# Kernel tuning notes

Hardware: AMD Instinct MI355X
Metric: run time of the kernel (lower is better)

The kernel has to match this reference:

```python
import jax, jax.numpy as jnp
import numpy as np

STATE_DIM = 128
ACT_DIM = 32
ENC_K = 10   # encoder_spine_dim
DEC_K = 10   # decoder_dim
H0, H1 = 2048, 2048
BATCH = 16384
MAX_ACTION = 1.0
STD0 = 0.3872983346207417  # sqrt(0.15)


def setup_inputs() -> dict:
    key = jax.random.key(0)
    ks = jax.random.split(key, 10)
    state = jax.random.normal(ks[0], (BATCH, STATE_DIM), dtype=jnp.float32)
    # encoder params: mean linspace over mean_range, std constant
    mean_enc = jnp.broadcast_to(jnp.linspace(-3.0, 3.0, ENC_K, dtype=jnp.float32),
                                (1, STATE_DIM, ENC_K))
    std_enc = jnp.full((1, STATE_DIM, ENC_K), STD0, dtype=jnp.float32)
    def lin(k, fan_in, fan_out):
        bound = 1.0 / np.sqrt(fan_in)
        k1, k2 = jax.random.split(k)
        W = jax.random.uniform(k1, (fan_out, fan_in), jnp.float32, -bound, bound)
        b = jax.random.uniform(k2, (fan_out,), jnp.float32, -bound, bound)
        return W, b
    W1, b1 = lin(ks[1], STATE_DIM * ENC_K, H0)
    W2, b2 = lin(ks[2], H0, H1)
    W3, b3 = lin(ks[3], H1, ACT_DIM * DEC_K)
    # grouped conv1d: weight [act_dim, 1, dec_k], bias [act_dim]
    bound = 1.0 / np.sqrt(DEC_K)
    Wd = jax.random.uniform(ks[4], (ACT_DIM, 1, DEC_K), jnp.float32, -bound, bound)
    bd = jax.random.uniform(ks[5], (ACT_DIM,), jnp.float32, -bound, bound)
    return {"state": state, "mean_enc": mean_enc, "std_enc": std_enc,
            "W1": W1, "b1": b1, "W2": W2, "b2": b2, "W3": W3, "b3": b3,
            "Wd": Wd, "bd": bd}


def reference(state, mean_enc, std_enc, W1, b1, W2, b2, W3, b3, Wd, bd):
    # Population-coding encoder: sigmoid((obs - mean)/std), flattened
    spine = jax.nn.sigmoid((state[:, :, None] - mean_enc) / std_enc)  # [B, D, K]
    spine = spine.reshape(state.shape[0], -1)                         # [B, D*K]
    a = jax.nn.relu(spine @ W1.T + b1)
    a = jax.nn.relu(a @ W2.T + b2)
    a = a @ W3.T + b3                                                 # [B, A*Kd]
    d = a.reshape(-1, ACT_DIM, DEC_K)                                 # [B, A, Kd]
    # grouped Conv1d with kernel == length => per-channel dot product
    raw = jnp.einsum('bak,ak->ba', d, Wd[:, 0, :]) + bd               # [B, A]
    return MAX_ACTION * jnp.tanh(raw)
```

## Files before the change

kernel.cpp:

```cpp
#include <hip/hip_runtime.h>
#include <hip/hip_bf16.h>
#include <stdint.h>

#define BATCH   16384
#define SDIM    128
#define ENCK    10
#define ADIM    32
#define DECK    10
#define HID     2048
#define KSPINE  1280

typedef __bf16 bf16x8 __attribute__((ext_vector_type(8)));
typedef float  f32x4  __attribute__((ext_vector_type(4)));

typedef __attribute__((address_space(1))) const void kGlobalVoid;
typedef __attribute__((address_space(3))) void       kLdsVoid;

__device__ __forceinline__ unsigned short f2b(float f) {
  union { float f; unsigned u; } v; v.f = f;
  unsigned r = v.u + 0x7fffu + ((v.u >> 16) & 1u);
  return (unsigned short)(r >> 16);
}

__global__ void f2b_kernel(const float* __restrict__ in, unsigned* __restrict__ out, int n2) {
  int i = blockIdx.x * blockDim.x + threadIdx.x;
  if (i >= n2) return;
  float2 v = reinterpret_cast<const float2*>(in)[i];
  out[i] = (unsigned)f2b(v.x) | ((unsigned)f2b(v.y) << 16);
}

__global__ __launch_bounds__(256) void encoder_kernel(const float* __restrict__ state,
                               const float* __restrict__ mean,
                               const float* __restrict__ stdv,
                               unsigned* __restrict__ spine) {
  int idx = blockIdx.x * 256 + threadIdx.x;
  int idx1 = (int)(((long long)idx * 0x66666667LL) >> 33);
  int kk = idx - idx1 * 5;
  int d  = idx1 & (SDIM - 1);
  float x = state[idx1];
  int mi = d * ENCK + kk * 2;
  float m0 = mean[mi], m1 = mean[mi + 1];
  float s0 = stdv[mi], s1 = stdv[mi + 1];
  float v0 = 1.f / (1.f + __expf((m0 - x) / s0));
  float v1 = 1.f / (1.f + __expf((m1 - x) / s1));
  spine[idx] = (unsigned)f2b(v0) | ((unsigned)f2b(v1) << 16);
}

__global__ void weff_kernel(const float* __restrict__ W3, const float* __restrict__ Wd,
                            unsigned short* __restrict__ Weff) {
  int idx = blockIdx.x * 256 + threadIdx.x;
  int a = idx >> 11, j = idx & 2047;
  float s = 0.f;
#pragma unroll
  for (int k = 0; k < DECK; ++k)
    s += Wd[a * DECK + k] * W3[(size_t)(a * DECK + k) * HID + j];
  Weff[idx] = f2b(s);
}

__global__ void beff_kernel(const float* __restrict__ b3, const float* __restrict__ Wd,
                            const float* __restrict__ bd, float* __restrict__ beff) {
  int a = threadIdx.x;
  if (a >= ADIM) return;
  float s = bd[a];
#pragma unroll
  for (int k = 0; k < DECK; ++k) s += Wd[a * DECK + k] * b3[a * DECK + k];
  beff[a] = s;
}


#define A0B 0
#define B0B 32768
#define A1B 65536
#define B1B 98304

#define FENCE asm volatile("" ::: "memory")

#define STAGE(BASEPTR, R0A, R0B, LDS0, LDS1, KT)                                             \
  __builtin_amdgcn_global_load_lds((kGlobalVoid*)((BASEPTR) + (size_t)((R0A) + rs) * K + (KT) + ce), \
                                   (kLdsVoid*)(smem + (LDS0) + t * 16), 16, 0, 0);           \
  __builtin_amdgcn_global_load_lds((kGlobalVoid*)((BASEPTR) + (size_t)((R0B) + rs) * K + (KT) + ce), \
                                   (kLdsVoid*)(smem + (LDS1) + t * 16), 16, 0, 0);

#define DS_AF(DST, ABASE, MPN)                                                               \
  _Pragma("unroll")                                                                          \
  for (int j2 = 0; j2 < 2; ++j2) {                                                           \
    _Pragma("unroll")                                                                        \
    for (int ks = 0; ks < 2; ++ks) {                                                         \
      int rowl = wr * 128 + (MPN) * 32 + j2 * 16 + lr;                                       \
      DST[j2][ks] = *reinterpret_cast<const bf16x8*>(                                        \
          smem + (ABASE) + rowl * 128 + ((((ks) << 6) | (kh << 4)) ^ swz));                  \
    }                                                                                        \
  }

#define DS_B2(DST, NP, BBASE)                                                                \
  _Pragma("unroll")                                                                          \
  for (int ks = 0; ks < 2; ++ks) {                                                           \
    int rowl = wc * 64 + (NP) * 16 + lr;                                                     \
    DST[NP][ks] = *reinterpret_cast<const bf16x8*>(                                          \
        smem + (BBASE) + rowl * 128 + ((((ks) << 6) | (kh << 4)) ^ swz));                    \
  }

#define DS_BF(DST, BBASE)                                                                    \
  _Pragma("unroll")                                                                          \
  for (int n = 0; n < 4; ++n) {                                                              \
    _Pragma("unroll")                                                                        \
    for (int ks = 0; ks < 2; ++ks) {                                                         \
      int rowl = wc * 64 + n * 16 + lr;                                                      \
      DST[n][ks] = *reinterpret_cast<const bf16x8*>(                                         \
          smem + (BBASE) + rowl * 128 + ((((ks) << 6) | (kh << 4)) ^ swz));                  \
    }                                                                                        \
  }

#define MFMA16(MP, AF, BF)                                                                   \
  _Pragma("unroll")                                                                          \
  for (int j2 = 0; j2 < 2; ++j2)                                                             \
    _Pragma("unroll")                                                                        \
    for (int n = 0; n < 4; ++n)                                                              \
      _Pragma("unroll")                                                                      \
      for (int ks = 0; ks < 2; ++ks)                                                         \
        acc[(MP) * 2 + j2][n] = __builtin_amdgcn_mfma_f32_16x16x32_bf16(                     \
            AF[j2][ks], BF[n][ks], acc[(MP) * 2 + j2][n], 0, 0, 0);

#define SGB_PHASE                                                                            \
  __builtin_amdgcn_sched_group_barrier(0x8, 2, 0);                                           \
  __builtin_amdgcn_sched_group_barrier(0x100, 1, 0);                                         \
  __builtin_amdgcn_sched_group_barrier(0x8, 2, 0);                                           \
  __builtin_amdgcn_sched_group_barrier(0x100, 1, 0);                                         \
  __builtin_amdgcn_sched_group_barrier(0x20, 2, 0);                                          \
  __builtin_amdgcn_sched_group_barrier(0x8, 3, 0);                                           \
  __builtin_amdgcn_sched_group_barrier(0x100, 1, 0);                                         \
  __builtin_amdgcn_sched_group_barrier(0x8, 3, 0);                                           \
  __builtin_amdgcn_sched_group_barrier(0x100, 1, 0);                                         \
  __builtin_amdgcn_sched_group_barrier(0x8, 3, 0);                                           \
  __builtin_amdgcn_sched_group_barrier(0x100, 1, 0);                                         \
  __builtin_amdgcn_sched_group_barrier(0x8, 3, 0);                                           \
  __builtin_amdgcn_sched_group_barrier(0x100, 1, 0);

#define VM_NONE
#define VM2 asm volatile("s_waitcnt vmcnt(2)" ::: "memory"); __builtin_amdgcn_sched_barrier(0);
#define VM6 asm volatile("s_waitcnt vmcnt(6)" ::: "memory"); __builtin_amdgcn_sched_barrier(0);

#define PH(MP, AF_C, AF_N, BF_C, BF_N, NXT_A, NXT_MP, BBASE_N, VMW, STG)                     \
  do {                                                                                       \
    asm volatile("s_waitcnt lgkmcnt(0)" ::: "memory");                                       \
    __builtin_amdgcn_sched_barrier(0);                                                       \
    VMW                                                                                      \
    __builtin_amdgcn_s_setprio(1);                                                           \
    MFMA16(MP, AF_C, BF_C);                                                                  \
    __builtin_amdgcn_s_setprio(0);                                                           \
    DS_AF(AF_N, NXT_A, NXT_MP);                                                              \
    DS_B2(BF_N, MP, BBASE_N);                                                                \
    STG;                                                                                     \
    SGB_PHASE;                                                                               \
    FENCE;                                                                                   \
    __builtin_amdgcn_s_barrier();                                                            \
  } while (0)

__global__ __launch_bounds__(512, 2) void gemm256(
    const unsigned short* __restrict__ A,
    const unsigned short* __restrict__ Bw,
    const float* __restrict__ bias,
    unsigned short* __restrict__ Cout,
    int K, int NI) {
  __shared__ char smem[131072];

  const int t    = threadIdx.x;
  const int lane = t & 63;
  const int w    = t >> 6;
  const int wr   = w >> 2;
  const int wc   = w & 3;
  const int lr   = lane & 15;
  const int kh   = lane >> 4;
  const int swz  = (lr & 7) << 4;
  const int rs   = t >> 3;
  const int ce   = ((t & 7) ^ (rs & 7)) << 3;

  const int bid = blockIdx.x;
  const int xcd = bid & 7, idx = bid >> 3;
  const int row0 = (xcd * 8 + (idx >> 3)) * 256;
  const int col0 = (idx & 7) * 256;

  f32x4 acc[8][4];
#pragma unroll
  for (int m = 0; m < 8; ++m)
#pragma unroll
    for (int n = 0; n < 4; ++n)
      acc[m][n] = (f32x4){0.f, 0.f, 0.f, 0.f};

  bf16x8 afc[2][2], afn[2][2], bfA[4][2], bfB[4][2];

  STAGE(Bw, col0 + 0,   col0 + 64,  B0B + 0,     B0B + 8192,  0);
  STAGE(Bw, col0 + 128, col0 + 192, B0B + 16384, B0B + 24576, 0);
  STAGE(A,  row0 + 0,   row0 + 128, A0B + 0,     A0B + 16384, 0);
  STAGE(A,  row0 + 64,  row0 + 192, A0B + 8192,  A0B + 24576, 0);
  STAGE(Bw, col0 + 0,   col0 + 64,  B1B + 0,     B1B + 8192,  64);
  STAGE(Bw, col0 + 128, col0 + 192, B1B + 16384, B1B + 24576, 64);
  STAGE(A,  row0 + 0,   row0 + 128, A1B + 0,     A1B + 16384, 64);
  asm volatile("s_waitcnt vmcnt(0)" ::: "memory");
  FENCE;
  __builtin_amdgcn_s_barrier();
  DS_AF(afc, A0B, 0);
  DS_BF(bfA, B0B);

  for (int i = 0; i < NI; ++i) {
    int kt0 = i << 7;
    int kt1 = kt0 + 64;
    int kt2 = kt0 + 128; if (kt2 >= K) kt2 -= K;
    int kt3 = kt0 + 192; if (kt3 >= K) kt3 -= K;

    PH(0, afc, afn, bfA, bfB, A0B, 1, B1B, VM2,
       STAGE(A,  row0 + 64,  row0 + 192, A1B + 8192,  A1B + 24576, kt1));
    PH(1, afn, afc, bfA, bfB, A0B, 2, B1B, VM_NONE,
       STAGE(Bw, col0 + 0,   col0 + 64,  B0B + 0,     B0B + 8192,  kt2));
    PH(2, afc, afn, bfA, bfB, A0B, 3, B1B, VM_NONE,
       STAGE(Bw, col0 + 128, col0 + 192, B0B + 16384, B0B + 24576, kt2));
    PH(3, afn, afc, bfA, bfB, A1B, 0, B1B, VM6,
       STAGE(A,  row0 + 0,   row0 + 128, A0B + 0,     A0B + 16384, kt2));
    PH(0, afc, afn, bfB, bfA, A1B, 1, B0B, VM2,
       STAGE(A,  row0 + 64,  row0 + 192, A0B + 8192,  A0B + 24576, kt2));
    PH(1, afn, afc, bfB, bfA, A1B, 2, B0B, VM_NONE,
       STAGE(Bw, col0 + 0,   col0 + 64,  B1B + 0,     B1B + 8192,  kt3));
    PH(2, afc, afn, bfB, bfA, A1B, 3, B0B, VM_NONE,
       STAGE(Bw, col0 + 128, col0 + 192, B1B + 16384, B1B + 24576, kt3));
    PH(3, afn, afc, bfB, bfA, A0B, 0, B0B, VM6,
       STAGE(A,  row0 + 0,   row0 + 128, A1B + 0,     A1B + 16384, kt3));
  }

#pragma unroll
  for (int m = 0; m < 8; ++m) {
    int gr0 = row0 + wr * 128 + m * 16 + kh * 4;
#pragma unroll
    for (int n = 0; n < 4; ++n) {
      int gc = col0 + wc * 64 + n * 16 + lr;
      float bv = bias[gc];
#pragma unroll
      for (int v = 0; v < 4; ++v) {
        float val = fmaxf(acc[m][n][v] + bv, 0.f);
        Cout[(size_t)(gr0 + v) * 2048 + gc] = f2b(val);
      }
    }
  }
}

__global__ __launch_bounds__(256) void gemm_skinny(
    const unsigned short* __restrict__ A,
    const unsigned short* __restrict__ Bw,
    const float* __restrict__ beff,
    float* __restrict__ out) {
  __shared__ char red[6144];
  const int t = threadIdx.x, lane = t & 63, w = t >> 6;
  const int lr = lane & 15, kh = lane >> 4;
  const int row0 = blockIdx.x * 16;
  const int kb = w * (HID / 4);
  f32x4 acc[2];
  acc[0] = (f32x4){0.f, 0.f, 0.f, 0.f};
  acc[1] = (f32x4){0.f, 0.f, 0.f, 0.f};

  const unsigned short* Arow = A  + (size_t)(row0 + lr) * HID + kb + kh * 8;
  const unsigned short* B0   = Bw + (size_t)(lr) * HID + kb + kh * 8;
  const unsigned short* B1   = Bw + (size_t)(16 + lr) * HID + kb + kh * 8;

#pragma unroll 4
  for (int kt = 0; kt < HID / 4; kt += 32) {
    bf16x8 a  = *reinterpret_cast<const bf16x8*>(Arow + kt);
    bf16x8 b0 = *reinterpret_cast<const bf16x8*>(B0 + kt);
    bf16x8 b1 = *reinterpret_cast<const bf16x8*>(B1 + kt);
    acc[0] = __builtin_amdgcn_mfma_f32_16x16x32_bf16(a, b0, acc[0], 0, 0, 0);
    acc[1] = __builtin_amdgcn_mfma_f32_16x16x32_bf16(a, b1, acc[1], 0, 0, 0);
  }

  if (w) {
    char* p = red + (w - 1) * 2048 + lane * 32;
    *reinterpret_cast<f32x4*>(p)      = acc[0];
    *reinterpret_cast<f32x4*>(p + 16) = acc[1];
  }
  __syncthreads();
  if (w == 0) {
#pragma unroll
    for (int j = 0; j < 3; ++j) {
      char* p = red + j * 2048 + lane * 32;
      acc[0] += *reinterpret_cast<const f32x4*>(p);
      acc[1] += *reinterpret_cast<const f32x4*>(p + 16);
    }
#pragma unroll
    for (int n = 0; n < 2; ++n)
#pragma unroll
      for (int v = 0; v < 4; ++v) {
        int row = row0 + kh * 4 + v;
        int col = n * 16 + lr;
        out[(size_t)row * ADIM + col] = tanhf(acc[n][v] + beff[col]);
      }
  }
}

extern "C" void kernel_launch(void* const* d_in, const int* in_sizes, int n_in,
                              void* d_out, int out_size, void* d_ws, size_t ws_size,
                              hipStream_t stream) {
  const float* state    = (const float*)d_in[0];
  const float* mean_enc = (const float*)d_in[1];
  const float* std_enc  = (const float*)d_in[2];
  const float* W1 = (const float*)d_in[3];
  const float* b1 = (const float*)d_in[4];
  const float* W2 = (const float*)d_in[5];
  const float* b2 = (const float*)d_in[6];
  const float* W3 = (const float*)d_in[7];
  const float* b3 = (const float*)d_in[8];
  const float* Wd = (const float*)d_in[9];
  const float* bd = (const float*)d_in[10];

  char* ws = (char*)d_ws;
  unsigned short* W1b   = (unsigned short*)(ws + 0);
  unsigned short* W2b   = (unsigned short*)(ws + 5242880);
  unsigned short* Weff  = (unsigned short*)(ws + 13631488);
  float*          beff  = (float*)(ws + 13762560);
  unsigned short* spine = (unsigned short*)(ws + 13762688);
  unsigned short* h1    = (unsigned short*)(ws + 55705728);
  unsigned short* h2    = (unsigned short*)(ws + 122814592);

  f2b_kernel<<<5120, 256, 0, stream>>>(W1, (unsigned*)W1b, 1310720);
  f2b_kernel<<<8192, 256, 0, stream>>>(W2, (unsigned*)W2b, 2097152);
  weff_kernel<<<256, 256, 0, stream>>>(W3, Wd, Weff);
  beff_kernel<<<1, 64, 0, stream>>>(b3, Wd, bd, beff);

  encoder_kernel<<<(BATCH * SDIM * 5) / 256, 256, 0, stream>>>(state, mean_enc, std_enc, (unsigned*)spine);

  gemm256<<<512, 512, 0, stream>>>(spine, W1b, b1, h1, KSPINE, KSPINE / 128);
  gemm256<<<512, 512, 0, stream>>>(h1,    W2b, b2, h2, HID,    HID / 128);
  gemm_skinny<<<BATCH / 16, 256, 0, stream>>>(h2, Weff, beff, (float*)d_out);
}
```

Measured before the change: 249.9 us.

## Fuse population encoder into first GEMM and merge prep kernels into one launch

The separate encoder kernel that materialised a 42MB bf16 spine buffer is removed. The first GEMM now computes sigmoid activations on the fly from state and a precomputed per-column scale/offset table, writing them straight into LDS in place of the async global-to-LDS loads. The four weight preparation kernels are merged into a single launch. This removes the spine write and read traffic and several launch overheads, but adds transcendental math and scalar state loads inside the GEMM pipeline, which can stall MFMA issue and changes the wait scheduling.

```diff
diff --git a/kernel.cpp b/kernel.cpp
--- a/kernel.cpp
+++ b/kernel.cpp
@@ -9,6 +9,7 @@
 #define DECK    10
 #define HID     2048
 #define KSPINE  1280
+#define L2E     1.4426950408889634f
 
 typedef __bf16 bf16x8 __attribute__((ext_vector_type(8)));
 typedef float  f32x4  __attribute__((ext_vector_type(4)));
@@ -22,51 +23,47 @@
   return (unsigned short)(r >> 16);
 }
 
-__global__ void f2b_kernel(const float* __restrict__ in, unsigned* __restrict__ out, int n2) {
-  int i = blockIdx.x * blockDim.x + threadIdx.x;
-  if (i >= n2) return;
-  float2 v = reinterpret_cast<const float2*>(in)[i];
-  out[i] = (unsigned)f2b(v.x) | ((unsigned)f2b(v.y) << 16);
-}
-
-__global__ __launch_bounds__(256) void encoder_kernel(const float* __restrict__ state,
-                               const float* __restrict__ mean,
-                               const float* __restrict__ stdv,
-                               unsigned* __restrict__ spine) {
-  int idx = blockIdx.x * 256 + threadIdx.x;
-  int idx1 = (int)(((long long)idx * 0x66666667LL) >> 33);
-  int kk = idx - idx1 * 5;
-  int d  = idx1 & (SDIM - 1);
-  float x = state[idx1];
-  int mi = d * ENCK + kk * 2;
-  float m0 = mean[mi], m1 = mean[mi + 1];
-  float s0 = stdv[mi], s1 = stdv[mi + 1];
-  float v0 = 1.f / (1.f + __expf((m0 - x) / s0));
-  float v1 = 1.f / (1.f + __expf((m1 - x) / s1));
-  spine[idx] = (unsigned)f2b(v0) | ((unsigned)f2b(v1) << 16);
-}
-
-__global__ void weff_kernel(const float* __restrict__ W3, const float* __restrict__ Wd,
-                            unsigned short* __restrict__ Weff) {
-  int idx = blockIdx.x * 256 + threadIdx.x;
-  int a = idx >> 11, j = idx & 2047;
-  float s = 0.f;
-#pragma unroll
-  for (int k = 0; k < DECK; ++k)
-    s += Wd[a * DECK + k] * W3[(size_t)(a * DECK + k) * HID + j];
-  Weff[idx] = f2b(s);
-}
-
-__global__ void beff_kernel(const float* __restrict__ b3, const float* __restrict__ Wd,
-                            const float* __restrict__ bd, float* __restrict__ beff) {
-  int a = threadIdx.x;
-  if (a >= ADIM) return;
-  float s = bd[a];
-#pragma unroll
-  for (int k = 0; k < DECK; ++k) s += Wd[a * DECK + k] * b3[a * DECK + k];
-  beff[a] = s;
-}
-
+__global__ __launch_bounds__(256) void prep_kernel(
+    const float* __restrict__ W1, const float* __restrict__ W2,
+    const float* __restrict__ W3, const float* __restrict__ Wd,
+    const float* __restrict__ b3, const float* __restrict__ bd,
+    const float* __restrict__ mean, const float* __restrict__ stdv,
+    unsigned* __restrict__ W1b, unsigned* __restrict__ W2b,
+    unsigned short* __restrict__ Weff, float* __restrict__ beff,
+    float2* __restrict__ ab_tab) {
+  int b = blockIdx.x, t = threadIdx.x;
+  if (b < 5120) {
+    int i = b * 256 + t;
+    float2 v = reinterpret_cast<const float2*>(W1)[i];
+    W1b[i] = (unsigned)f2b(v.x) | ((unsigned)f2b(v.y) << 16);
+  } else if (b < 13312) {
+    int i = (b - 5120) * 256 + t;
+    float2 v = reinterpret_cast<const float2*>(W2)[i];
+    W2b[i] = (unsigned)f2b(v.x) | ((unsigned)f2b(v.y) << 16);
+  } else if (b < 13568) {
+    int idx = (b - 13312) * 256 + t;
+    int a = idx >> 11, j = idx & 2047;
+    float s = 0.f;
+#pragma unroll
+    for (int k = 0; k < DECK; ++k)
+      s += Wd[a * DECK + k] * W3[(size_t)(a * DECK + k) * HID + j];
+    Weff[idx] = f2b(s);
+  } else {
+    if (t < ADIM) {
+      float s = bd[t];
+#pragma unroll
+      for (int k = 0; k < DECK; ++k) s += Wd[t * DECK + k] * b3[t * DECK + k];
+      beff[t] = s;
+    }
+#pragma unroll
+    for (int e = 0; e < 5; ++e) {
+      int i = e * 256 + t;
+      float sd = stdv[i], m = mean[i];
+      float2 ab; ab.x = -L2E / sd; ab.y = L2E * m / sd;
+      ab_tab[i] = ab;
+    }
+  }
+}
 
 #define A0B 0
 #define B0B 32768
@@ -74,6 +71,9 @@
 #define B1B 98304
 
 #define FENCE asm volatile("" ::: "memory")
+#define SB0 __builtin_amdgcn_sched_barrier(0)
+#define BAR __builtin_amdgcn_s_barrier()
+#define LGKM0 do { asm volatile("s_waitcnt lgkmcnt(0)" ::: "memory"); SB0; } while (0)
 
 #define STAGE(BASEPTR, R0A, R0B, LDS0, LDS1, KT)                                             \
   __builtin_amdgcn_global_load_lds((kGlobalVoid*)((BASEPTR) + (size_t)((R0A) + rs) * K + (KT) + ce), \
@@ -120,6 +120,47 @@
       for (int ks = 0; ks < 2; ++ks)                                                         \
         acc[(MP) * 2 + j2][n] = __builtin_amdgcn_mfma_f32_16x16x32_bf16(                     \
             AF[j2][ks], BF[n][ks], acc[(MP) * 2 + j2][n], 0, 0, 0);
+
+#define GEMM_HEAD                                                                            \
+  __shared__ char smem[131072];                                                              \
+  const int t    = threadIdx.x;                                                              \
+  const int lane = t & 63;                                                                   \
+  const int w    = t >> 6;                                                                   \
+  const int wr   = w >> 2;                                                                   \
+  const int wc   = w & 3;                                                                    \
+  const int lr   = lane & 15;                                                                \
+  const int kh   = lane >> 4;                                                                \
+  const int swz  = (lr & 7) << 4;                                                            \
+  const int rs   = t >> 3;                                                                   \
+  const int ce   = ((t & 7) ^ (rs & 7)) << 3;                                                \
+  const int bid = blockIdx.x;                                                                \
+  const int xcd = bid & 7, idx = bid >> 3;                                                   \
+  const int row0 = (xcd * 8 + (idx >> 3)) * 256;                                             \
+  const int col0 = (idx & 7) * 256;                                                          \
+  f32x4 acc[8][4];                                                                           \
+  _Pragma("unroll")                                                                          \
+  for (int m = 0; m < 8; ++m)                                                                \
+    _Pragma("unroll")                                                                        \
+    for (int n = 0; n < 4; ++n)                                                              \
+      acc[m][n] = (f32x4){0.f, 0.f, 0.f, 0.f};                                               \
+  bf16x8 afc[2][2], afn[2][2], bfA[4][2], bfB[4][2];
+
+#define GEMM_EPILOGUE(RELUQ)                                                                 \
+  _Pragma("unroll")                                                                          \
+  for (int m = 0; m < 8; ++m) {                                                              \
+    int gr0 = row0 + wr * 128 + m * 16 + kh * 4;                                             \
+    _Pragma("unroll")                                                                        \
+    for (int n = 0; n < 4; ++n) {                                                            \
+      int gc = col0 + wc * 64 + n * 16 + lr;                                                 \
+      float bv = bias[gc];                                                                   \
+      _Pragma("unroll")                                                                      \
+      for (int v = 0; v < 4; ++v) {                                                          \
+        float val = acc[m][n][v] + bv;                                                       \
+        if (RELUQ) val = fmaxf(val, 0.f);                                                    \
+        Cout[(size_t)(gr0 + v) * 2048 + gc] = f2b(val);                                      \
+      }                                                                                      \
+    }                                                                                        \
+  }
 
 #define SGB_PHASE                                                                            \
   __builtin_amdgcn_sched_group_barrier(0x8, 2, 0);                                           \
@@ -137,13 +178,12 @@
   __builtin_amdgcn_sched_group_barrier(0x100, 1, 0);
 
 #define VM_NONE
-#define VM2 asm volatile("s_waitcnt vmcnt(2)" ::: "memory"); __builtin_amdgcn_sched_barrier(0);
-#define VM6 asm volatile("s_waitcnt vmcnt(6)" ::: "memory"); __builtin_amdgcn_sched_barrier(0);
+#define VM2 asm volatile("s_waitcnt vmcnt(2)" ::: "memory"); SB0;
+#define VM6 asm volatile("s_waitcnt vmcnt(6)" ::: "memory"); SB0;
 
 #define PH(MP, AF_C, AF_N, BF_C, BF_N, NXT_A, NXT_MP, BBASE_N, VMW, STG)                     \
   do {                                                                                       \
-    asm volatile("s_waitcnt lgkmcnt(0)" ::: "memory");                                       \
-    __builtin_amdgcn_sched_barrier(0);                                                       \
+    LGKM0;                                                                                   \
     VMW                                                                                      \
     __builtin_amdgcn_s_setprio(1);                                                           \
     MFMA16(MP, AF_C, BF_C);                                                                  \
@@ -153,41 +193,14 @@
     STG;                                                                                     \
     SGB_PHASE;                                                                               \
     FENCE;                                                                                   \
-    __builtin_amdgcn_s_barrier();                                                            \
+    BAR;                                                                                     \
   } while (0)
 
 __global__ __launch_bounds__(512, 2) void gemm256(
-    const unsigned short* __restrict__ A,
-    const unsigned short* __restrict__ Bw,
-    const float* __restrict__ bias,
-    unsigned short* __restrict__ Cout,
+    const unsigned short* __restrict__ A, const unsigned short* __restrict__ Bw,
+    const float* __restrict__ bias, unsigned short* __restrict__ Cout,
     int K, int NI) {
-  __shared__ char smem[131072];
-
-  const int t    = threadIdx.x;
-  const int lane = t & 63;
-  const int w    = t >> 6;
-  const int wr   = w >> 2;
-  const int wc   = w & 3;
-  const int lr   = lane & 15;
-  const int kh   = lane >> 4;
-  const int swz  = (lr & 7) << 4;
-  const int rs   = t >> 3;
-  const int ce   = ((t & 7) ^ (rs & 7)) << 3;
-
-  const int bid = blockIdx.x;
-  const int xcd = bid & 7, idx = bid >> 3;
-  const int row0 = (xcd * 8 + (idx >> 3)) * 256;
-  const int col0 = (idx & 7) * 256;
-
-  f32x4 acc[8][4];
-#pragma unroll
-  for (int m = 0; m < 8; ++m)
-#pragma unroll
-    for (int n = 0; n < 4; ++n)
-      acc[m][n] = (f32x4){0.f, 0.f, 0.f, 0.f};
-
-  bf16x8 afc[2][2], afn[2][2], bfA[4][2], bfB[4][2];
+  GEMM_HEAD
 
   STAGE(Bw, col0 + 0,   col0 + 64,  B0B + 0,     B0B + 8192,  0);
   STAGE(Bw, col0 + 128, col0 + 192, B0B + 16384, B0B + 24576, 0);
@@ -197,8 +210,7 @@
   STAGE(Bw, col0 + 128, col0 + 192, B1B + 16384, B1B + 24576, 64);
   STAGE(A,  row0 + 0,   row0 + 128, A1B + 0,     A1B + 16384, 64);
   asm volatile("s_waitcnt vmcnt(0)" ::: "memory");
-  FENCE;
-  __builtin_amdgcn_s_barrier();
+  FENCE; BAR;
   DS_AF(afc, A0B, 0);
   DS_BF(bfA, B0B);
 
@@ -225,28 +237,109 @@
     PH(3, afn, afc, bfB, bfA, A0B, 0, B0B, VM6,
        STAGE(A,  row0 + 0,   row0 + 128, A1B + 0,     A1B + 16384, kt3));
   }
-
-#pragma unroll
-  for (int m = 0; m < 8; ++m) {
-    int gr0 = row0 + wr * 128 + m * 16 + kh * 4;
-#pragma unroll
-    for (int n = 0; n < 4; ++n) {
-      int gc = col0 + wc * 64 + n * 16 + lr;
-      float bv = bias[gc];
-#pragma unroll
-      for (int v = 0; v < 4; ++v) {
-        float val = fmaxf(acc[m][n][v] + bv, 0.f);
-        Cout[(size_t)(gr0 + v) * 2048 + gc] = f2b(val);
-      }
-    }
-  }
+  GEMM_EPILOGUE(true)
+}
+
+
+#define ENC_ROW(SV0, SV1, PK)                                                                \
+  _Pragma("unroll")                                                                          \
+  for (int jj = 0; jj < 4; ++jj) {                                                           \
+    float s0 = ((c0 + 2 * jj)     >= t10) ? SV1 : SV0;                                       \
+    float s1 = ((c0 + 2 * jj + 1) >= t10) ? SV1 : SV0;                                       \
+    float v0 = __builtin_amdgcn_rcpf(                                                        \
+        1.f + __builtin_amdgcn_exp2f(fmaf(s0, abv[2 * jj].x, abv[2 * jj].y)));               \
+    float v1 = __builtin_amdgcn_rcpf(                                                        \
+        1.f + __builtin_amdgcn_exp2f(fmaf(s1, abv[2 * jj + 1].x, abv[2 * jj + 1].y)));       \
+    PK[jj] = (unsigned)f2b(v0) | ((unsigned)f2b(v1) << 16);                                  \
+  }
+
+#define ENC_STAGE(R0A, R0B, LDS0, LDS1, KT)                                                  \
+  do {                                                                                       \
+    int c0 = (KT) + ce;                                                                      \
+    float2 abv[8];                                                                           \
+    _Pragma("unroll")                                                                        \
+    for (int jj = 0; jj < 8; ++jj) abv[jj] = ab_tab[c0 + jj];                                \
+    int d0 = (c0 * 6554) >> 16;                                                              \
+    int t10 = (d0 + 1) * 10;                                                                 \
+    int d1 = d0 + 1; if (d1 > 127) d1 = 127;                                                 \
+    float sA0 = state[(size_t)((R0A) + rs) * SDIM + d0];                                     \
+    float sA1 = state[(size_t)((R0A) + rs) * SDIM + d1];                                     \
+    float sB0 = state[(size_t)((R0B) + rs) * SDIM + d0];                                     \
+    float sB1 = state[(size_t)((R0B) + rs) * SDIM + d1];                                     \
+    unsigned pa[4], pb[4];                                                                   \
+    ENC_ROW(sA0, sA1, pa)                                                                    \
+    ENC_ROW(sB0, sB1, pb)                                                                    \
+    *reinterpret_cast<uint4*>(smem + (LDS0) + t * 16) = make_uint4(pa[0], pa[1], pa[2], pa[3]); \
+    *reinterpret_cast<uint4*>(smem + (LDS1) + t * 16) = make_uint4(pb[0], pb[1], pb[2], pb[3]); \
+  } while (0)
+
+#define VM0F asm volatile("s_waitcnt vmcnt(0)" ::: "memory"); SB0;
+
+#define PH1(MP, AF_C, AF_N, BF_C, BF_N, NXT_A, NXT_MP, BBASE_N, DOVM, STG)                   \
+  do {                                                                                       \
+    LGKM0;                                                                                   \
+    __builtin_amdgcn_s_setprio(1);                                                           \
+    MFMA16(MP, AF_C, BF_C);                                                                  \
+    __builtin_amdgcn_s_setprio(0);                                                           \
+    STG;                                                                                     \
+    DS_AF(AF_N, NXT_A, NXT_MP);                                                              \
+    DS_B2(BF_N, MP, BBASE_N);                                                                \
+    if (DOVM) { VM0F }                                                                       \
+    FENCE;                                                                                   \
+    BAR;                                                                                     \
+  } while (0)
+
+__global__ __launch_bounds__(512, 2) void gemm1f(
+    const float* __restrict__ state,
+    const unsigned short* __restrict__ Bw,
+    const float* __restrict__ bias,
+    unsigned short* __restrict__ Cout,
+    const float2* __restrict__ ab_tab) {
+  const int K = KSPINE, NI = KSPINE / 128;
+  GEMM_HEAD
+
+  STAGE(Bw, col0 + 0,   col0 + 64,  B0B + 0,     B0B + 8192,  0);
+  STAGE(Bw, col0 + 128, col0 + 192, B0B + 16384, B0B + 24576, 0);
+  ENC_STAGE(row0 + 0,  row0 + 128, A0B + 0,    A0B + 16384, 0);
+  ENC_STAGE(row0 + 64, row0 + 192, A0B + 8192, A0B + 24576, 0);
+  STAGE(Bw, col0 + 0,   col0 + 64,  B1B + 0,     B1B + 8192,  64);
+  STAGE(Bw, col0 + 128, col0 + 192, B1B + 16384, B1B + 24576, 64);
+  ENC_STAGE(row0 + 0,  row0 + 128, A1B + 0,    A1B + 16384, 64);
+  asm volatile("s_waitcnt vmcnt(0)" ::: "memory");
+  LGKM0;
+  FENCE; BAR;
+  DS_AF(afc, A0B, 0);
+  DS_BF(bfA, B0B);
+
+  for (int i = 0; i < NI; ++i) {
+    int kt0 = i << 7;
+    int kt1 = kt0 + 64;
+    int kt2 = kt0 + 128; if (kt2 >= K) kt2 -= K;
+    int kt3 = kt0 + 192; if (kt3 >= K) kt3 -= K;
+
+    PH1(0, afc, afn, bfA, bfB, A0B, 1, B1B, false,
+        ENC_STAGE(row0 + 64, row0 + 192, A1B + 8192, A1B + 24576, kt1));
+    PH1(1, afn, afc, bfA, bfB, A0B, 2, B1B, false,
+        STAGE(Bw, col0 + 0,   col0 + 64,  B0B + 0,     B0B + 8192,  kt2));
+    PH1(2, afc, afn, bfA, bfB, A0B, 3, B1B, false,
+        STAGE(Bw, col0 + 128, col0 + 192, B0B + 16384, B0B + 24576, kt2));
+    PH1(3, afn, afc, bfA, bfB, A1B, 0, B1B, true,
+        ENC_STAGE(row0 + 0, row0 + 128, A0B + 0, A0B + 16384, kt2));
+    PH1(0, afc, afn, bfB, bfA, A1B, 1, B0B, false,
+        ENC_STAGE(row0 + 64, row0 + 192, A0B + 8192, A0B + 24576, kt2));
+    PH1(1, afn, afc, bfB, bfA, A1B, 2, B0B, false,
+        STAGE(Bw, col0 + 0,   col0 + 64,  B1B + 0,     B1B + 8192,  kt3));
+    PH1(2, afc, afn, bfB, bfA, A1B, 3, B0B, false,
+        STAGE(Bw, col0 + 128, col0 + 192, B1B + 16384, B1B + 24576, kt3));
+    PH1(3, afn, afc, bfB, bfA, A0B, 0, B0B, true,
+        ENC_STAGE(row0 + 0, row0 + 128, A1B + 0, A1B + 16384, kt3));
+  }
+  GEMM_EPILOGUE(true)
 }
 
 __global__ __launch_bounds__(256) void gemm_skinny(
-    const unsigned short* __restrict__ A,
-    const unsigned short* __restrict__ Bw,
-    const float* __restrict__ beff,
-    float* __restrict__ out) {
+    const unsigned short* __restrict__ A, const unsigned short* __restrict__ Bw,
+    const float* __restrict__ beff, float* __restrict__ out) {
   __shared__ char red[6144];
   const int t = threadIdx.x, lane = t & 63, w = t >> 6;
   const int lr = lane & 15, kh = lane >> 4;
@@ -309,22 +402,17 @@
   const float* bd = (const float*)d_in[10];
 
   char* ws = (char*)d_ws;
-  unsigned short* W1b   = (unsigned short*)(ws + 0);
-  unsigned short* W2b   = (unsigned short*)(ws + 5242880);
+  unsigned*       W1b   = (unsigned*)(ws + 0);
+  unsigned*       W2b   = (unsigned*)(ws + 5242880);
   unsigned short* Weff  = (unsigned short*)(ws + 13631488);
   float*          beff  = (float*)(ws + 13762560);
-  unsigned short* spine = (unsigned short*)(ws + 13762688);
-  unsigned short* h1    = (unsigned short*)(ws + 55705728);
-  unsigned short* h2    = (unsigned short*)(ws + 122814592);
-
-  f2b_kernel<<<5120, 256, 0, stream>>>(W1, (unsigned*)W1b, 1310720);
-  f2b_kernel<<<8192, 256, 0, stream>>>(W2, (unsigned*)W2b, 2097152);
-  weff_kernel<<<256, 256, 0, stream>>>(W3, Wd, Weff);
-  beff_kernel<<<1, 64, 0, stream>>>(b3, Wd, bd, beff);
-
-  encoder_kernel<<<(BATCH * SDIM * 5) / 256, 256, 0, stream>>>(state, mean_enc, std_enc, (unsigned*)spine);
-
-  gemm256<<<512, 512, 0, stream>>>(spine, W1b, b1, h1, KSPINE, KSPINE / 128);
-  gemm256<<<512, 512, 0, stream>>>(h1,    W2b, b2, h2, HID,    HID / 128);
+  float2*         ab_tab= (float2*)(ws + 13762688);
+  unsigned short* h1    = (unsigned short*)(ws + 13772928);
+  unsigned short* h2    = (unsigned short*)(ws + 80881792);
+
+  prep_kernel<<<13569, 256, 0, stream>>>(W1, W2, W3, Wd, b3, bd, mean_enc, std_enc,
+                                         W1b, W2b, Weff, beff, ab_tab);
+  gemm1f<<<512, 512, 0, stream>>>(state, (const unsigned short*)W1b, b1, h1, ab_tab);
+  gemm256<<<512, 512, 0, stream>>>(h1, (const unsigned short*)W2b, b2, h2, HID, HID / 128);
   gemm_skinny<<<BATCH / 16, 256, 0, stream>>>(h2, Weff, beff, (float*)d_out);
 }
```

After: 283.3 us. +13.4%, slower.
